# Kernel optimization log

Hardware: AMD Instinct MI355X
Metric: run time of the kernel (lower is better)

## Reference

```python
import jax, jax.numpy as jnp
import numpy as np
from jax import lax

B, H, W, CL, CC, CD, NH, NP = 8, 48, 48, 384, 384, 384, 12, 4
N = H * W
HD = CL // NH
SCALE = HD ** -0.5


def _pool_mat(n, out=7):
    # torch AdaptiveAvgPool2d bin edges: [floor(i*n/out), ceil((i+1)*n/out))
    M = np.zeros((out, n), np.float32)
    for i in range(out):
        s = (i * n) // out
        e = -(-((i + 1) * n) // out)
        M[i, s:e] = 1.0 / (e - s)
    return jnp.asarray(M)


def _resize_mat(out_n, in_n):
    # bilinear, align_corners=False (torch F.interpolate)
    M = np.zeros((out_n, in_n), np.float32)
    scale = in_n / out_n
    for o in range(out_n):
        src = (o + 0.5) * scale - 0.5
        src = min(max(src, 0.0), in_n - 1.0)
        i0 = int(np.floor(src))
        i1 = min(i0 + 1, in_n - 1)
        f = src - i0
        M[o, i0] += 1.0 - f
        M[o, i1] += f
    return jnp.asarray(M)


def _ln_c(x, g, b):
    # LayerNorm over channel dim of NCHW, eps=1e-6
    mu = jnp.mean(x, axis=1, keepdims=True)
    var = jnp.mean((x - mu) ** 2, axis=1, keepdims=True)
    xn = (x - mu) * lax.rsqrt(var + 1e-6)
    return xn * g[None, :, None, None] + b[None, :, None, None]


def _c1(x, w):
    # 1x1 conv, w: (out,in)
    return jnp.einsum('oc,bchw->bohw', w, x)


def _bilerp(feat, grid):
    # feat (G,C,Hs,Ws), grid (G,M,2) xy in [-1,1]; align_corners=False, zero padding
    G, C, Hs, Ws = feat.shape
    x = (grid[..., 0] + 1.0) * 0.5 * Ws - 0.5
    y = (grid[..., 1] + 1.0) * 0.5 * Hs - 0.5
    x0 = jnp.floor(x)
    y0 = jnp.floor(y)
    fx = x - x0
    fy = y - y0
    featf = feat.transpose(0, 2, 3, 1).reshape(G, Hs * Ws, C)
    x0i = x0.astype(jnp.int32)
    y0i = y0.astype(jnp.int32)

    def corner(ix, iy):
        valid = ((ix >= 0) & (ix < Ws) & (iy >= 0) & (iy < Hs)).astype(feat.dtype)
        flat = jnp.clip(iy, 0, Hs - 1) * Ws + jnp.clip(ix, 0, Ws - 1)
        g = jax.vmap(lambda f, i: f[i])(featf, flat)  # (G,M,C)
        return g * valid[..., None]

    v00 = corner(x0i, y0i)
    v01 = corner(x0i + 1, y0i)
    v10 = corner(x0i, y0i + 1)
    v11 = corner(x0i + 1, y0i + 1)
    w00 = ((1 - fx) * (1 - fy))[..., None]
    w01 = (fx * (1 - fy))[..., None]
    w10 = ((1 - fx) * fy)[..., None]
    w11 = (fx * fy)[..., None]
    return v00 * w00 + v01 * w01 + v10 * w10 + v11 * w11  # (G,M,C)


def _forward(local_feat, context_prior, deformable_x, W_q, W_k, W_v, W_pre, ln1_g, ln1_b,
             W_post, dw_w, dw_b, ln2_g, ln2_b, W_lo, b_lo, W_off, b_off,
             attention_biases, W_p, bn_g, bn_b, bn_mean, bn_var):
    q = _c1(local_feat, W_q)  # (B,CL,H,W)

    # context_offset_guide: 1x1 -> GELU -> adaptive pool 7x7 -> LN(C) -> 1x1 to 32 -> resize
    cg = jax.nn.gelu(_c1(context_prior, W_pre), approximate=False)
    Mh, Mw = _pool_mat(H), _pool_mat(W)
    pooled = jnp.einsum('oh,pw,bchw->bcop', Mh, Mw, cg)
    guide = _c1(_ln_c(pooled, ln1_g, ln1_b), W_post)  # (B,32,7,7)
    Uh, Uw = _resize_mat(H, 7), _resize_mat(W, 7)
    guide = jnp.einsum('Oh,Pw,bchw->bcOP', Uh, Uw, guide)  # (B,32,H,W)

    # local_offset_base: dwconv3x3 -> LN(C) -> GELU -> 1x1 to 32
    dw = lax.conv_general_dilated(local_feat, dw_w, (1, 1), [(1, 1), (1, 1)],
                                  dimension_numbers=('NCHW', 'OIHW', 'NCHW'),
                                  feature_group_count=CL) + dw_b[None, :, None, None]
    lo = jax.nn.gelu(_ln_c(dw, ln2_g, ln2_b), approximate=False)
    lo = _c1(lo, W_lo) + b_lo[None, :, None, None]  # (B,32,H,W)

    fused = jnp.concatenate([guide, lo], axis=1)  # (B,64,H,W)
    off = _c1(fused, W_off) + b_off[None, :, None, None]  # (B,NH*NP*2,H,W)
    off = off.transpose(0, 2, 3, 1).reshape(B, H, W, NH, NP, 2)
    offn = off / jnp.asarray([W, H], dtype=off.dtype)

    ry = (jnp.arange(H, dtype=off.dtype) + 0.5) / H
    rx = (jnp.arange(W, dtype=off.dtype) + 0.5) / W
    ref = jnp.stack([jnp.broadcast_to(rx[None, :], (H, W)),
                     jnp.broadcast_to(ry[:, None], (H, W))], axis=-1)  # (H,W,2) xy
    grid = (ref[None, :, :, None, None, :] + offn) * 2.0 - 1.0  # (B,H,W,NH,NP,2)

    gridh = grid.reshape(B, N, NH, NP, 2).transpose(0, 2, 1, 3, 4)  # (B,NH,N,NP,2)
    grid_r = gridh.reshape(B * NH, N * NP, 2)

    k = _c1(context_prior, W_k).reshape(B * NH, HD, H, W)
    v = _c1(deformable_x, W_v).reshape(B * NH, HD, H, W)
    k_s = _bilerp(k, grid_r).reshape(B, NH, N, NP, HD)
    v_s = _bilerp(v, grid_r).reshape(B, NH, N, NP, HD)

    qh = q.reshape(B, NH, HD, N).transpose(0, 1, 3, 2)  # (B,NH,N,HD)
    scores = jnp.einsum('bhnd,bhnpd->bhnp', qh, k_s) * SCALE

    # relative position bias: idx(p1,p2) = |dy|*W + |dx| (first-seen enumeration)
    px = jnp.clip(jnp.round((gridh[..., 0] + 1.0) * 0.5 * W - 0.5), 0, W - 1).astype(jnp.int32)
    py = jnp.clip(jnp.round((gridh[..., 1] + 1.0) * 0.5 * H - 0.5), 0, H - 1).astype(jnp.int32)
    n = jnp.arange(N, dtype=jnp.int32)
    qy = (n // W)[None, None, :, None]
    qx = (n % W)[None, None, :, None]
    bidx = jnp.abs(qy - py) * W + jnp.abs(qx - px)  # (B,NH,N,NP)
    bias = attention_biases[jnp.arange(NH)[None, :, None, None], bidx]

    attn = jax.nn.softmax(scores + bias, axis=-1)
    out = jnp.einsum('bhnp,bhnpd->bhnd', attn, v_s)  # (B,NH,N,HD)
    out = out.transpose(0, 1, 3, 2).reshape(B, CL, H, W)

    y = _c1(out, W_p)
    y = bn_g[None, :, None, None] * (y - bn_mean[None, :, None, None]) * \
        lax.rsqrt(bn_var[None, :, None, None] + 1e-5) + bn_b[None, :, None, None]
    return y


def setup_inputs():
    ks = jax.random.split(jax.random.key(0), 16)
    f32 = jnp.float32
    d = {
        'local_feat': jax.random.normal(ks[0], (B, CL, H, W), f32),
        'context_prior': jax.random.normal(ks[1], (B, CC, H, W), f32),
        'deformable_x': jax.random.normal(ks[2], (B, CD, H, W), f32),
        'W_q': jax.random.normal(ks[3], (CL, CL), f32) * 0.02,
        'W_k': jax.random.normal(ks[4], (CL, CC), f32) * 0.02,
        'W_v': jax.random.normal(ks[5], (CD, CD), f32) * 0.02,
        'W_pre': jax.random.normal(ks[6], (CC, CC), f32) * 0.02,
        'ln1_g': jnp.ones((CC,), f32),
        'ln1_b': jnp.zeros((CC,), f32),
        'W_post': jax.random.normal(ks[7], (32, CC), f32) * 0.02,
        'dw_w': jax.random.normal(ks[8], (CL, 1, 3, 3), f32) * 0.1,
        'dw_b': jnp.zeros((CL,), f32),
        'ln2_g': jnp.ones((CL,), f32),
        'ln2_b': jnp.zeros((CL,), f32),
        'W_lo': jax.random.normal(ks[9], (32, CL), f32) * 0.02,
        'b_lo': jnp.zeros((32,), f32),
        'W_off': jax.random.normal(ks[10], (NH * NP * 2, 64), f32) * 0.01,
        'b_off': jax.random.normal(ks[11], (NH * NP * 2,), f32) * 0.5,
        'attention_biases': jax.random.normal(ks[12], (NH, H * W), f32) * 0.02,
        'W_p': jax.random.normal(ks[13], (CL, CL), f32) * 0.02,
        'bn_g': jnp.ones((CL,), f32),
        'bn_b': jnp.zeros((CL,), f32),
        'bn_mean': jax.random.normal(ks[14], (CL,), f32) * 0.01,
        'bn_var': jax.random.uniform(ks[15], (CL,), f32, 0.5, 1.5),
    }
    return d


def reference(local_feat, context_prior, deformable_x, W_q, W_k, W_v, W_pre, ln1_g, ln1_b,
              W_post, dw_w, dw_b, ln2_g, ln2_b, W_lo, b_lo, W_off, b_off,
              attention_biases, W_p, bn_g, bn_b, bn_mean, bn_var):
    return _forward(local_feat, context_prior, deformable_x, W_q, W_k, W_v, W_pre, ln1_g,
                    ln1_b, W_post, dw_w, dw_b, ln2_g, ln2_b, W_lo, b_lo, W_off, b_off,
                    attention_biases, W_p, bn_g, bn_b, bn_mean, bn_var)
```

## Files before the change

### kernel.cpp

```cpp
#include <hip/hip_runtime.h>
#include <hip/hip_bf16.h>
#include <math.h>

#define B_ 8
#define H_ 48
#define W_ 48
#define N_ 2304
#define C_ 384
#define NH_ 12
#define NP_ 4
#define HD_ 32
#define SCALE_ 0.17677669529663687f

typedef unsigned short ushort;
typedef short bf16x8 __attribute__((ext_vector_type(8)));
typedef float f32x4 __attribute__((ext_vector_type(4)));

__device__ __forceinline__ float b2f(ushort u) {
    union { float f; unsigned i; } x; x.i = ((unsigned)u) << 16; return x.f;
}
__device__ __forceinline__ ushort f2b(float f) {
    __hip_bfloat16 h = __float2bfloat16(f);
    return *(ushort*)&h;
}
__device__ __forceinline__ float ldin(const void* p, size_t i, int isbf) {
    return isbf ? b2f(((const ushort*)p)[i]) : ((const float*)p)[i];
}
__device__ __forceinline__ float geluf(float x) {
    return 0.5f * x * (1.0f + erff(x * 0.70710678118654752440f));
}
__device__ __forceinline__ int iabs(int x) { return x < 0 ? -x : x; }
__device__ __forceinline__ int get_isbf(const void* lnq) {
    return (*(const unsigned*)lnq == 0x3F803F80u) ? 1 : 0;
}

__device__ __forceinline__ void gl_lds16(const ushort* g, ushort* l) {
    __builtin_amdgcn_global_load_lds(
        (const __attribute__((address_space(1))) unsigned int*)g,
        (__attribute__((address_space(3))) unsigned int*)l, 16, 0, 0);
}

#define PREP_MAX 24
struct PrepTab {
    const void* src[PREP_MAX];
    void*       dst[PREP_MAX];
    int         n[PREP_MAX];
    int         tobf[PREP_MAX];
};
struct TPtrs { const void* src[3]; ushort* dst[3]; };
struct SetupRaw {
    const void* WoffRaw;
    const void* WloRaw;
    const void* bloRaw;
    const void* boffRaw;
    const void* dwRaw;
    const void* lnq;
    ushort* Bext;
    float*  biasp;
    float*  dwwT;
};

__global__ __launch_bounds__(256) void setup_kernel(TPtrs tp, PrepTab tab, int ne, SetupRaw rw)
{
    const int isbf = get_isbf(rw.lnq);
    const int tid = threadIdx.x;
    const int bid = blockIdx.x;
    const int DWT0 = ne * 8;
    const int WC0  = DWT0 + 2;
    const int T30  = WC0 + 96;

    if (bid < DWT0) {
        const int e = bid >> 3, sub = bid & 7;
        const int n = tab.n[e];
        const void* src = tab.src[e];
        if (tab.tobf[e]) {
            ushort* dst = (ushort*)tab.dst[e];
            if (isbf) {
                const ushort* s = (const ushort*)src;
                for (int i = sub * 256 + tid; i < n; i += 8 * 256) dst[i] = s[i];
            } else {
                const float* s = (const float*)src;
                for (int i = sub * 256 + tid; i < n; i += 8 * 256) dst[i] = f2b(s[i]);
            }
        } else {
            float* dst = (float*)tab.dst[e];
            if (isbf) {
                const ushort* s = (const ushort*)src;
                for (int i = sub * 256 + tid; i < n; i += 8 * 256) dst[i] = b2f(s[i]);
            } else {
                const float* s = (const float*)src;
                for (int i = sub * 256 + tid; i < n; i += 8 * 256) dst[i] = s[i];
            }
        }
    } else if (bid < WC0) {
        const int c = (bid - DWT0) * 256 + tid;
        if (c < C_) {
#pragma unroll
            for (int u = 0; u < 9; u++)
                rw.dwwT[u * C_ + c] = ldin(rw.dwRaw, (size_t)c * 9 + u, isbf);
        }
    } else if (bid < T30) {
        const int co = bid - WC0;
        const ushort* WoffU = (const ushort*)rw.WoffRaw;
        for (int c = tid; c < C_; c += 256) {
            float acc = 0.f;
#pragma unroll 8
            for (int j = 0; j < 32; j++)
                acc += ldin(rw.WoffRaw, (size_t)co * 64 + 32 + j, isbf)
                     * ldin(rw.WloRaw, (size_t)j * 384 + c, isbf);
            ushort hi = f2b(acc);
            float r = acc - b2f(hi);
            ushort lo = f2b(r);
            rw.Bext[co * 1152 + c] = hi;
            rw.Bext[co * 1152 + 384 + c] = lo;
            rw.Bext[co * 1152 + 768 + c] = hi;
        }
        (void)WoffU;
        if (tid == 0) {
            float bp = ldin(rw.boffRaw, co, isbf);
            for (int j = 0; j < 32; j++)
                bp += ldin(rw.WoffRaw, (size_t)co * 64 + 32 + j, isbf)
                    * ldin(rw.bloRaw, j, isbf);
            rw.biasp[co] = bp;
        }
    } else {
        const int t3 = bid - T30;
        const int x = t3 % 36;
        const int rem = t3 / 36;
        const int y = rem % 12;
        const int z = rem / 12;
        const int which = z >> 3;
        const int b = z & 7;
        const int n0 = x * 64, c0 = y * 32;
        const void* in = tp.src[which];
        ushort* out = tp.dst[which];
        const int t = tid;

        __shared__ unsigned tile[64][33];

        if (isbf) {
            {
                const int c = t >> 3, s = t & 7;
                uint4 v = *(const uint4*)((const ushort*)in + ((size_t)b * C_ + c0 + c) * N_ + n0 + s * 8);
                const int nb = s * 8;
                tile[nb + 0][c] = v.x & 0xffff; tile[nb + 1][c] = v.x >> 16;
                tile[nb + 2][c] = v.y & 0xffff; tile[nb + 3][c] = v.y >> 16;
                tile[nb + 4][c] = v.z & 0xffff; tile[nb + 5][c] = v.z >> 16;
                tile[nb + 6][c] = v.w & 0xffff; tile[nb + 7][c] = v.w >> 16;
            }
            __syncthreads();
            {
                const int n = t >> 2, s = t & 3;
                const int cb = s * 8;
                unsigned p0 = tile[n][cb + 0] | (tile[n][cb + 1] << 16);
                unsigned p1 = tile[n][cb + 2] | (tile[n][cb + 3] << 16);
                unsigned p2 = tile[n][cb + 4] | (tile[n][cb + 5] << 16);
                unsigned p3 = tile[n][cb + 6] | (tile[n][cb + 7] << 16);
                uint4 o; o.x = p0; o.y = p1; o.z = p2; o.w = p3;
                *(uint4*)(out + ((size_t)b * N_ + n0 + n) * C_ + c0 + cb) = o;
            }
        } else {
            float* tf = (float*)&tile[0][0];
            const int tx = t & 31, ty = t >> 5;
            for (int sub = 0; sub < 2; sub++) {
                int ns = n0 + sub * 32;
                __syncthreads();
#pragma unroll
                for (int u = 0; u < 4; u++) {
                    int c = ty + u * 8;
                    tf[c * 33 + tx] = ((const float*)in)[((size_t)b * C_ + c0 + c) * N_ + ns + tx];
                }
                __syncthreads();
#pragma unroll
                for (int u = 0; u < 4; u++) {
                    int n = ty + u * 8;
                    out[((size_t)b * N_ + ns + n) * C_ + c0 + tx] = f2b(tf[tx * 33 + n]);
                }
            }
        }
    }
}

struct QKV4Ptrs { const ushort* A[4]; const ushort* Bw[4]; void* Y[4]; };
__global__ __launch_bounds__(256, 5) void mega_gemm_kernel(
    QKV4Ptrs qp,
    const ushort* __restrict__ AHI, const ushort* __restrict__ ALO,
    const ushort* __restrict__ Bext, float* __restrict__ OFFP)
{
    __shared__ ushort As[2][128 * 32];
    __shared__ ushort Bs[2][128 * 32];
    const int tid = threadIdx.x;
    const int lane = tid & 63, wave = tid >> 6;
    const int wr = wave >> 1, wc = wave & 1;
    const int quad = lane >> 4, l15 = lane & 15;
    const int bid = blockIdx.x;

    if (bid < 432) {
        const int seg = bid % 3;
        const int m0 = (bid / 3) * 128;
        const ushort* Ag = (seg < 2) ? AHI : ALO;
        const int bcol0 = seg * 384;

        f32x4 acc[4][3];
#pragma unroll
        for (int i = 0; i < 4; i++)
#pragma unroll
            for (int j = 0; j < 3; j++) acc[i][j] = (f32x4){0.f, 0.f, 0.f, 0.f};

        auto stage = [&](int p, int kc) {
#pragma unroll
            for (int u = 0; u < 2; u++) {
                int idx = tid + 256 * u;
                int r = idx >> 2, s = idx & 3;
                int rb = r < 96 ? r : 95;
                gl_lds16(Ag + (size_t)(m0 + r) * 384 + kc + 8 * s, &As[p][idx * 8]);
                gl_lds16(Bext + (size_t)rb * 1152 + bcol0 + kc + 8 * s, &Bs[p][idx * 8]);
            }
        };

        stage(0, 0);
        const int nt = 12;
        for (int t = 0; t < nt; ++t) {
            if (t + 1 < nt) {
                stage((t + 1) & 1, (t + 1) * 32);
                asm volatile("s_waitcnt vmcnt(4)" ::: "memory");
            } else {
                asm volatile("s_waitcnt vmcnt(0)" ::: "memory");
            }
            __builtin_amdgcn_s_barrier();
            __builtin_amdgcn_sched_barrier(0);
            const int p = t & 1;
            bf16x8 af[4], bfr[3];
#pragma unroll
            for (int i = 0; i < 4; i++)
                af[i]  = *(const bf16x8*)&As[p][(wr * 64 + i * 16 + l15) * 32 + quad * 8];
#pragma unroll
            for (int j = 0; j < 3; j++)
                bfr[j] = *(const bf16x8*)&Bs[p][(wc * 48 + j * 16 + l15) * 32 + quad * 8];
#pragma unroll
            for (int i = 0; i < 4; i++)
#pragma unroll
                for (int j = 0; j < 3; j++)
                    acc[i][j] = __builtin_amdgcn_mfma_f32_16x16x32_bf16(af[i], bfr[j], acc[i][j], 0, 0, 0);
            __builtin_amdgcn_s_barrier();
        }

        float* out = OFFP + (size_t)seg * ((size_t)B_ * N_ * 96);
#pragma unroll
        for (int i = 0; i < 4; i++) {
#pragma unroll
            for (int r = 0; r < 4; r++) {
                int m = m0 + wr * 64 + i * 16 + quad * 4 + r;
#pragma unroll
                for (int j = 0; j < 3; j++) {
                    int co = wc * 48 + j * 16 + l15;
                    out[(size_t)m * 96 + co] = acc[i][j][r];
                }
            }
        }
    } else {
        const int q = bid - 432;
        const int zc = q / 54, r2 = q % 54;
        const int which = zc >> 3, b = zc & 7;
        const int m0 = (r2 / 3) * 128;
        const int n0 = (r2 % 3) * 128;
        const ushort* Ag = qp.A[which];
        const ushort* Bg = qp.Bw[which];

        f32x4 acc[4][4];
#pragma unroll
        for (int i = 0; i < 4; i++)
#pragma unroll
            for (int j = 0; j < 4; j++) acc[i][j] = (f32x4){0.f, 0.f, 0.f, 0.f};

        const size_t abase = (size_t)b * (size_t)N_ * C_;

        auto stage = [&](int p, int kc) {
#pragma unroll
            for (int u = 0; u < 2; u++) {
                int idx = tid + 256 * u;
                int r = idx >> 2, s = idx & 3;
                gl_lds16(Ag + abase + (size_t)(m0 + r) * C_ + kc + 8 * s, &As[p][idx * 8]);
                gl_lds16(Bg + (size_t)(n0 + r) * C_ + kc + 8 * s, &Bs[p][idx * 8]);
            }
        };

        stage(0, 0);
        const int nt = C_ / 32;
        for (int t = 0; t < nt; ++t) {
            if (t + 1 < nt) {
                stage((t + 1) & 1, (t + 1) * 32);
                asm volatile("s_waitcnt vmcnt(4)" ::: "memory");
            } else {
                asm volatile("s_waitcnt vmcnt(0)" ::: "memory");
            }
            __builtin_amdgcn_s_barrier();
            __builtin_amdgcn_sched_barrier(0);
            const int p = t & 1;
            bf16x8 af[4], bfr[4];
#pragma unroll
            for (int i = 0; i < 4; i++)
                af[i]  = *(const bf16x8*)&As[p][(wr * 64 + i * 16 + l15) * 32 + quad * 8];
#pragma unroll
            for (int j = 0; j < 4; j++)
                bfr[j] = *(const bf16x8*)&Bs[p][(wc * 64 + j * 16 + l15) * 32 + quad * 8];
#pragma unroll
            for (int i = 0; i < 4; i++)
#pragma unroll
                for (int j = 0; j < 4; j++)
                    acc[i][j] = __builtin_amdgcn_mfma_f32_16x16x32_bf16(af[i], bfr[j], acc[i][j], 0, 0, 0);
            __builtin_amdgcn_s_barrier();
        }

        if (which < 3) {
            ushort* Yg = (ushort*)qp.Y[which];
#pragma unroll
            for (int i = 0; i < 4; i++) {
#pragma unroll
                for (int r = 0; r < 4; r++) {
                    int m = m0 + wr * 64 + i * 16 + quad * 4 + r;
#pragma unroll
                    for (int j = 0; j < 4; j++) {
                        int nn = n0 + wc * 64 + j * 16 + l15;
                        Yg[abase + (size_t)m * C_ + nn] = f2b(acc[i][j][r]);
                    }
                }
            }
        } else {
            float* Yg = (float*)qp.Y[3];
#pragma unroll
            for (int i = 0; i < 4; i++) {
#pragma unroll
                for (int r = 0; r < 4; r++) {
                    int m = m0 + wr * 64 + i * 16 + quad * 4 + r;
#pragma unroll
                    for (int j = 0; j < 4; j++) {
                        int nn = n0 + wc * 64 + j * 16 + l15;
                        Yg[abase + (size_t)m * C_ + nn] = geluf(acc[i][j][r]);
                    }
                }
            }
        }
    }
}

__global__ __launch_bounds__(256) void gemm_final_kernel(
    const ushort* __restrict__ WpB, const ushort* __restrict__ AOut,
    void* __restrict__ Yg,
    const float* __restrict__ bng, const float* __restrict__ bnb,
    const float* __restrict__ bnm, const float* __restrict__ bnv,
    const void* __restrict__ lnq)
{
    const int isbf = get_isbf(lnq);
    const int l = (blockIdx.x & 7) * 108 + (blockIdx.x >> 3);
    const int b = l / 108, r2 = l % 108;
    const int n0 = (r2 / 3) * 64;
    const int m0 = (r2 % 3) * 128;

    __shared__ ushort As[2][128 * 32];
    __shared__ ushort Bs[2][64 * 32];
    const int tid = threadIdx.x;
    const int lane = tid & 63, wave = tid >> 6;
    const int quad = lane >> 4, l15 = lane & 15;
    const int sx = (quad ^ (l15 & 3)) * 8;

    f32x4 acc[2][4];
#pragma unroll
    for (int i = 0; i < 2; i++)
#pragma unroll
        for (int j = 0; j < 4; j++) acc[i][j] = (f32x4){0.f, 0.f, 0.f, 0.f};

    const size_t bbase = (size_t)b * (size_t)N_ * C_;

    auto stage = [&](int p, int kc) {
#pragma unroll
        for (int u = 0; u < 2; u++) {
            int idx = tid + 256 * u;
            int r = idx >> 2, sl = idx & 3;
            int sg = sl ^ (r & 3);
            gl_lds16(WpB + (size_t)(m0 + r) * C_ + kc + 8 * sg, &As[p][idx * 8]);
        }
        {
            int r = tid >> 2, sl = tid & 3;
            int sg = sl ^ (r & 3);
            gl_lds16(AOut + bbase + (size_t)(n0 + r) * C_ + kc + 8 * sg, &Bs[p][tid * 8]);
        }
    };

    stage(0, 0);

    const int nt = C_ / 32;
    for (int t = 0; t < nt; ++t) {
        if (t + 1 < nt) {
            stage((t + 1) & 1, (t + 1) * 32);
            asm volatile("s_waitcnt vmcnt(3)" ::: "memory");
        } else {
            asm volatile("s_waitcnt vmcnt(0)" ::: "memory");
        }
        __builtin_amdgcn_s_barrier();
        __builtin_amdgcn_sched_barrier(0);
        const int p = t & 1;
        bf16x8 af[2], bfr[4];
#pragma unroll
        for (int i = 0; i < 2; i++)
            af[i]  = *(const bf16x8*)&As[p][(wave * 32 + i * 16 + l15) * 32 + sx];
#pragma unroll
        for (int j = 0; j < 4; j++)
            bfr[j] = *(const bf16x8*)&Bs[p][(j * 16 + l15) * 32 + sx];
#pragma unroll
        for (int i = 0; i < 2; i++)
#pragma unroll
            for (int j = 0; j < 4; j++)
                acc[i][j] = __builtin_amdgcn_mfma_f32_16x16x32_bf16(af[i], bfr[j], acc[i][j], 0, 0, 0);
        __builtin_amdgcn_s_barrier();
    }

    const size_t ybase = (size_t)b * (size_t)C_ * N_;
#pragma unroll
    for (int i = 0; i < 2; i++) {
#pragma unroll
        for (int r = 0; r < 4; r++) {
            int m = m0 + wave * 32 + i * 16 + quad * 4 + r;
            float sc = bng[m] * rsqrtf(bnv[m] + 1e-5f);
            float sh = bnb[m] - sc * bnm[m];
#pragma unroll
            for (int j = 0; j < 4; j++) {
                int nn = n0 + j * 16 + l15;
                float v = sc * acc[i][j][r] + sh;
                size_t yi = ybase + (size_t)m * N_ + nn;
                if (isbf) ((ushort*)Yg)[yi] = f2b(v);
                else ((float*)Yg)[yi] = v;
            }
        }
    }
}

__global__ __launch_bounds__(384) void pool_ln_guide_kernel(
    const float* __restrict__ CG, const float* __restrict__ g, const float* __restrict__ bt,
    const ushort* __restrict__ WpostB, const ushort* __restrict__ WoffB,
    float* __restrict__ OG7)
{
    const int cell = blockIdx.x % 49, b = blockIdx.x / 49;
    const int i = cell / 7, j = cell % 7, c = threadIdx.x;
    const int sh = (i * H_) / 7, eh = ((i + 1) * H_ + 6) / 7;
    const int sw = (j * W_) / 7, ew = ((j + 1) * W_ + 6) / 7;
    float s = 0.f;
    for (int h = sh; h < eh; h++)
        for (int w = sw; w < ew; w++)
            s += CG[((size_t)b * N_ + h * W_ + w) * C_ + c];
    s *= 1.0f / (float)((eh - sh) * (ew - sw));

    float rs = s, rq = s * s;
#pragma unroll
    for (int m = 1; m <= 32; m <<= 1) {
        rs += __shfl_xor(rs, m);
        rq += __shfl_xor(rq, m);
    }
    __shared__ float ss[6], sq[6], buf[C_];
    __shared__ float psum[12][33];
    __shared__ float g7s[32];
    int wid = threadIdx.x >> 6;
    if ((threadIdx.x & 63) == 0) { ss[wid] = rs; sq[wid] = rq; }
    __syncthreads();
    if (threadIdx.x == 0) {
        float ts = 0.f, tq = 0.f;
        for (int k = 0; k < 6; k++) { ts += ss[k]; tq += sq[k]; }
        ss[0] = ts; sq[0] = tq;
    }
    __syncthreads();
    float mu = ss[0] / (float)C_;
    float var = sq[0] / (float)C_ - mu * mu;
    float inv = rsqrtf(var + 1e-6f);
    buf[c] = (s - mu) * inv * g[c] + bt[c];
    __syncthreads();

    const int oc = threadIdx.x & 31, seg = threadIdx.x >> 5;
    const uint4* wp = (const uint4*)(WpostB + oc * C_ + seg * 32);
    float part = 0.f;
#pragma unroll
    for (int u = 0; u < 4; u++) {
        uint4 v = wp[u];
        const float* bb = &buf[seg * 32 + u * 8];
        part += b2f((ushort)(v.x & 0xffff)) * bb[0] + b2f((ushort)(v.x >> 16)) * bb[1];
        part += b2f((ushort)(v.y & 0xffff)) * bb[2] + b2f((ushort)(v.y >> 16)) * bb[3];
        part += b2f((ushort)(v.z & 0xffff)) * bb[4] + b2f((ushort)(v.z >> 16)) * bb[5];
        part += b2f((ushort)(v.w & 0xffff)) * bb[6] + b2f((ushort)(v.w >> 16)) * bb[7];
    }
    psum[seg][oc] = part;
    __syncthreads();
    if (threadIdx.x < 32) {
        float acc = 0.f;
#pragma unroll
        for (int k = 0; k < 12; k++) acc += psum[k][threadIdx.x];
        g7s[threadIdx.x] = acc;
    }
    __syncthreads();
    if (threadIdx.x < 96) {
        const int co = threadIdx.x;
        float acc = 0.f;
#pragma unroll 8
        for (int k = 0; k < 32; k++)
            acc += b2f(WoffB[co * 64 + k]) * g7s[k];
        OG7[(size_t)blockIdx.x * 96 + co] = acc;
    }
}

__global__ __launch_bounds__(512) void dw_ln_gelu_kernel(
    const ushort* __restrict__ LF, const float* __restrict__ WdT, const float* __restrict__ BdF,
    const float* __restrict__ g, const float* __restrict__ bt,
    ushort* __restrict__ AHI, ushort* __restrict__ ALO)
{
    const int wave = threadIdx.x >> 6, lane = threadIdx.x & 63;
    const int m = blockIdx.x * 8 + wave;
    const int b = m / N_, n = m % N_;
    const int h = n / W_, w = n % W_;
    const bool act = lane < 48;
    const int c0 = lane * 8;

    float acc[8];
#pragma unroll
    for (int j = 0; j < 8; j++) acc[j] = 0.f;
    if (act) {
        f32x4 b0 = *(const f32x4*)(BdF + c0);
        f32x4 b1 = *(const f32x4*)(BdF + c0 + 4);
#pragma unroll
        for (int j = 0; j < 4; j++) { acc[j] = b0[j]; acc[4 + j] = b1[j]; }
    }

#pragma unroll
    for (int u = 0; u < 9; u++) {
        const int ky = u / 3, kx = u % 3;
        const int y = h + ky - 1, x = w + kx - 1;
        if (act && y >= 0 && y < H_ && x >= 0 && x < W_) {
            uint4 v = *(const uint4*)(LF + ((size_t)b * N_ + y * W_ + x) * C_ + c0);
            f32x4 wa = *(const f32x4*)(WdT + u * C_ + c0);
            f32x4 wb = *(const f32x4*)(WdT + u * C_ + c0 + 4);
            acc[0] += wa[0] * b2f((ushort)(v.x & 0xffff));
            acc[1] += wa[1] * b2f((ushort)(v.x >> 16));
            acc[2] += wa[2] * b2f((ushort)(v.y & 0xffff));
            acc[3] += wa[3] * b2f((ushort)(v.y >> 16));
            acc[4] += wb[0] * b2f((ushort)(v.z & 0xffff));
            acc[5] += wb[1] * b2f((ushort)(v.z >> 16));
            acc[6] += wb[2] * b2f((ushort)(v.w & 0xffff));
            acc[7] += wb[3] * b2f((ushort)(v.w >> 16));
        }
    }

    float rs = 0.f, rq = 0.f;
#pragma unroll
    for (int j = 0; j < 8; j++) { rs += acc[j]; rq += acc[j] * acc[j]; }
#pragma unroll
    for (int s = 1; s <= 32; s <<= 1) {
        rs += __shfl_xor(rs, s);
        rq += __shfl_xor(rq, s);
    }
    float mu = rs / (float)C_;
    float var = rq / (float)C_ - mu * mu;
    float inv = rsqrtf(var + 1e-6f);

    if (act) {
        f32x4 g0 = *(const f32x4*)(g + c0);
        f32x4 g1 = *(const f32x4*)(g + c0 + 4);
        f32x4 t0 = *(const f32x4*)(bt + c0);
        f32x4 t1 = *(const f32x4*)(bt + c0 + 4);
        float v[8];
#pragma unroll
        for (int j = 0; j < 4; j++) {
            v[j]     = geluf((acc[j]     - mu) * inv * g0[j] + t0[j]);
            v[4 + j] = geluf((acc[4 + j] - mu) * inv * g1[j] + t1[j]);
        }
        uint4 hi, lo;
        ushort hs[8], ls[8];
#pragma unroll
        for (int j = 0; j < 8; j++) {
            hs[j] = f2b(v[j]);
            ls[j] = f2b(v[j] - b2f(hs[j]));
        }
        hi.x = (unsigned)hs[0] | ((unsigned)hs[1] << 16);
        hi.y = (unsigned)hs[2] | ((unsigned)hs[3] << 16);
        hi.z = (unsigned)hs[4] | ((unsigned)hs[5] << 16);
        hi.w = (unsigned)hs[6] | ((unsigned)hs[7] << 16);
        lo.x = (unsigned)ls[0] | ((unsigned)ls[1] << 16);
        lo.y = (unsigned)ls[2] | ((unsigned)ls[3] << 16);
        lo.z = (unsigned)ls[4] | ((unsigned)ls[5] << 16);
        lo.w = (unsigned)ls[6] | ((unsigned)ls[7] << 16);
        size_t idx = (size_t)m * C_ + c0;
        *(uint4*)(AHI + idx) = hi;
        *(uint4*)(ALO + idx) = lo;
    }
}

__global__ __launch_bounds__(384) void attn_kernel(
    const ushort* __restrict__ Q, const ushort* __restrict__ K, const ushort* __restrict__ V,
    const float* __restrict__ OFFP, const float* __restrict__ biasp,
    const float* __restrict__ OG7,
    const float* __restrict__ ABf, ushort* __restrict__ OUT)
{
    const int pairi = blockIdx.x;
    const int b = pairi / (N_ / 2);
    const int n0 = (pairi % (N_ / 2)) * 2;
    const int tid = threadIdx.x;

    __shared__ int   cidxS[96][4];
    __shared__ float cwS[96][4];
    __shared__ float biasS[96];

    if (tid < 96) {
        const int pos = tid / 48, idx = tid % 48;
        const int n = n0 + pos;
        const int h = n / W_, w = n % W_;
        const int nh = idx >> 2, p = idx & 3;
        const int co = nh * 8 + 2 * p;

        const float fs = 7.0f / 48.0f;
        float sy = fminf(fmaxf(((float)h + 0.5f) * fs - 0.5f, 0.f), 6.f);
        float sx = fminf(fmaxf(((float)w + 0.5f) * fs - 0.5f, 0.f), 6.f);
        int gy0 = (int)floorf(sy), gx0 = (int)floorf(sx);
        int gy1 = min(gy0 + 1, 6), gx1 = min(gx0 + 1, 6);
        float gfy = sy - (float)gy0, gfx = sx - (float)gx0;
        float bw00 = (1.f - gfy) * (1.f - gfx), bw01 = (1.f - gfy) * gfx;
        float bw10 = gfy * (1.f - gfx), bw11 = gfy * gfx;
        const float* ogb = OG7 + (size_t)b * 49 * 96;
        int c00 = (gy0 * 7 + gx0) * 96, c01 = (gy0 * 7 + gx1) * 96;
        int c10 = (gy1 * 7 + gx0) * 96, c11 = (gy1 * 7 + gx1) * 96;
        const size_t MS = (size_t)B_ * N_ * 96;
        const size_t mrow = ((size_t)b * N_ + n) * 96;

        float ox = OFFP[mrow + co] + OFFP[MS + mrow + co] + OFFP[2 * MS + mrow + co]
                 + biasp[co]
                 + bw00 * ogb[c00 + co] + bw01 * ogb[c01 + co]
                 + bw10 * ogb[c10 + co] + bw11 * ogb[c11 + co];
        float oy = OFFP[mrow + co + 1] + OFFP[MS + mrow + co + 1] + OFFP[2 * MS + mrow + co + 1]
                 + biasp[co + 1]
                 + bw00 * ogb[c00 + co + 1] + bw01 * ogb[c01 + co + 1]
                 + bw10 * ogb[c10 + co + 1] + bw11 * ogb[c11 + co + 1];

        float x = (float)w + ox;
        float y = (float)h + oy;

        int px = (int)fminf(fmaxf(rintf(x), 0.f), (float)(W_ - 1));
        int py = (int)fminf(fmaxf(rintf(y), 0.f), (float)(H_ - 1));
        biasS[tid] = ABf[(size_t)nh * N_ + iabs(h - py) * W_ + iabs(w - px)];

        float x0f = floorf(x), y0f = floorf(y);
        float fx = x - x0f, fy = y - y0f;
        int x0 = (int)x0f, y0 = (int)y0f;
#pragma unroll
        for (int cc = 0; cc < 4; cc++) {
            int dx = cc & 1, dy = cc >> 1;
            int ix = x0 + dx, iy = y0 + dy;
            bool valid = (ix >= 0) && (ix < W_) && (iy >= 0) && (iy < H_);
            int ixc = min(max(ix, 0), W_ - 1), iyc = min(max(iy, 0), H_ - 1);
            cidxS[tid][cc] = iyc * W_ + ixc;
            float wx = dx ? fx : (1.f - fx);
            float wy = dy ? fy : (1.f - fy);
            cwS[tid][cc] = valid ? wx * wy : 0.f;
        }
    }
    __syncthreads();

    const int pos = tid / 192, r = tid % 192;
    const int nh = r >> 4, dd = r & 15;
    const int n = n0 + pos;
    const size_t row = ((size_t)b * N_ + n) * C_ + nh * HD_ + dd * 2;
    unsigned qu = *(const unsigned*)(Q + row);
    const float q0 = b2f((ushort)(qu & 0xffff));
    const float q1 = b2f((ushort)(qu >> 16));
    const size_t kvbase = (size_t)b * N_ * C_ + nh * HD_ + dd * 2;
    const int s0 = pos * 48 + nh * 4;

    int   ci[NP_][4];
    float cw[NP_][4];
#pragma unroll
    for (int p = 0; p < NP_; p++)
#pragma unroll
        for (int cc = 0; cc < 4; cc++) {
            ci[p][cc] = cidxS[s0 + p][cc];
            cw[p][cc] = cwS[s0 + p][cc];
        }

    float sc[NP_];
#pragma unroll
    for (int p = 0; p < NP_; p++) {
        float ks0 = 0.f, ks1 = 0.f;
#pragma unroll
        for (int cc = 0; cc < 4; cc++) {
            unsigned kv = *(const unsigned*)(K + kvbase + (size_t)ci[p][cc] * C_);
            ks0 += cw[p][cc] * b2f((ushort)(kv & 0xffff));
            ks1 += cw[p][cc] * b2f((ushort)(kv >> 16));
        }
        float dot = q0 * ks0 + q1 * ks1;
#pragma unroll
        for (int m = 1; m <= 8; m <<= 1) dot += __shfl_xor(dot, m);
        sc[p] = dot * SCALE_ + biasS[s0 + p];
    }

    float m = fmaxf(fmaxf(sc[0], sc[1]), fmaxf(sc[2], sc[3]));
    float e[NP_], esum = 0.f;
#pragma unroll
    for (int p = 0; p < NP_; p++) { e[p] = __expf(sc[p] - m); esum += e[p]; }
    float inv = 1.0f / esum;

    float o0 = 0.f, o1 = 0.f;
#pragma unroll
    for (int p = 0; p < NP_; p++) {
        float vs0 = 0.f, vs1 = 0.f;
#pragma unroll
        for (int cc = 0; cc < 4; cc++) {
            unsigned vv = *(const unsigned*)(V + kvbase + (size_t)ci[p][cc] * C_);
            vs0 += cw[p][cc] * b2f((ushort)(vv & 0xffff));
            vs1 += cw[p][cc] * b2f((ushort)(vv >> 16));
        }
        float ep = e[p] * inv;
        o0 += ep * vs0;
        o1 += ep * vs1;
    }
    unsigned ou = (unsigned)f2b(o0) | ((unsigned)f2b(o1) << 16);
    *(unsigned*)(OUT + row) = ou;
}

extern "C" void kernel_launch(void* const* d_in, const int* in_sizes, int n_in,
                              void* d_out, int out_size, void* d_ws, size_t ws_size,
                              hipStream_t stream)
{
    const void* local_feat    = d_in[0];
    const void* context_prior = d_in[1];
    const void* deformable_x  = d_in[2];

    const size_t BIGE = (size_t)B_ * N_ * C_;

    char* wsb = (char*)d_ws;
    auto carve = [&](size_t bytes) { char* p = wsb; wsb += (bytes + 255) & ~(size_t)255; return p; };
    int*    flag = (int*)carve(256);
    ushort* T1   = (ushort*)carve(BIGE * 2);
    ushort* T2   = (ushort*)carve(BIGE * 2);
    ushort* T3   = (ushort*)carve(BIGE * 2);
    ushort* Qb   = (ushort*)carve(BIGE * 2);
    ushort* Kb   = (ushort*)carve(BIGE * 2);
    ushort* Vb   = (ushort*)carve(BIGE * 2);
    ushort* AHI  = (ushort*)carve(BIGE * 2);
    ushort* ALO  = (ushort*)carve(BIGE * 2);
    float*  CGR  = (float*)carve(BIGE * 4);
    float*  OFFB = (float*)carve((size_t)B_ * N_ * 96 * 4 * 3);
    ushort* WqB   = (ushort*)carve(147456 * 2);
    ushort* WkB   = (ushort*)carve(147456 * 2);
    ushort* WvB   = (ushort*)carve(147456 * 2);
    ushort* WpreB = (ushort*)carve(147456 * 2);
    ushort* WpB   = (ushort*)carve(147456 * 2);
    ushort* WpostB= (ushort*)carve(12288 * 2);
    ushort* WoffB = (ushort*)carve(6144 * 2);
    ushort* Bext  = (ushort*)carve(96 * 1152 * 2);
    float*  biasp = (float*)carve(96 * 4);
    float*  OG7   = (float*)carve((size_t)B_ * 49 * 96 * 4);
    float*  dwwT  = (float*)carve(3456 * 4);
    float*  ABf   = (float*)carve(27648 * 4);
    float*  dwbF  = (float*)carve(384 * 4);
    float*  ln1gF = (float*)carve(384 * 4);
    float*  ln1bF = (float*)carve(384 * 4);
    float*  ln2gF = (float*)carve(384 * 4);
    float*  ln2bF = (float*)carve(384 * 4);
    float*  bngF  = (float*)carve(384 * 4);
    float*  bnbF  = (float*)carve(384 * 4);
    float*  bnmF  = (float*)carve(384 * 4);
    float*  bnvF  = (float*)carve(384 * 4);
    ushort* AOut = (ushort*)CGR + BIGE;
    (void)flag;

    PrepTab tab;
    int ne = 0;
    auto add = [&](const void* s, void* d, int n, int tb) {
        tab.src[ne] = s; tab.dst[ne] = d; tab.n[ne] = n; tab.tobf[ne] = tb; ne++;
    };
    add(d_in[3],  WqB,   147456, 1);
    add(d_in[4],  WkB,   147456, 1);
    add(d_in[5],  WvB,   147456, 1);
    add(d_in[6],  WpreB, 147456, 1);
    add(d_in[19], WpB,   147456, 1);
    add(d_in[9],  WpostB, 12288, 1);
    add(d_in[16], WoffB,   6144, 1);
    add(d_in[18], ABf,    27648, 0);
    add(d_in[11], dwbF,     384, 0);
    add(d_in[7],  ln1gF,    384, 0);
    add(d_in[8],  ln1bF,    384, 0);
    add(d_in[12], ln2gF,    384, 0);
    add(d_in[13], ln2bF,    384, 0);
    add(d_in[20], bngF,     384, 0);
    add(d_in[21], bnbF,     384, 0);
    add(d_in[22], bnmF,     384, 0);
    add(d_in[23], bnvF,     384, 0);

    TPtrs tp;
    tp.src[0] = local_feat;    tp.dst[0] = T1;
    tp.src[1] = context_prior; tp.dst[1] = T2;
    tp.src[2] = deformable_x;  tp.dst[2] = T3;

    SetupRaw rw;
    rw.WoffRaw = d_in[16];
    rw.WloRaw  = d_in[14];
    rw.bloRaw  = d_in[15];
    rw.boffRaw = d_in[17];
    rw.dwRaw   = d_in[10];
    rw.lnq     = d_in[7];
    rw.Bext    = Bext;
    rw.biasp   = biasp;
    rw.dwwT    = dwwT;

    const int setup_blocks = ne * 8 + 2 + 96 + 10368;
    setup_kernel<<<setup_blocks, 256, 0, stream>>>(tp, tab, ne, rw);

    dim3 blk256(256);

    dw_ln_gelu_kernel<<<(B_ * N_) / 8, 512, 0, stream>>>(T1, dwwT, dwbF, ln2gF, ln2bF, AHI, ALO);

    QKV4Ptrs qp;
    qp.A[0] = T1; qp.Bw[0] = WqB;   qp.Y[0] = Qb;
    qp.A[1] = T2; qp.Bw[1] = WkB;   qp.Y[1] = Kb;
    qp.A[2] = T3; qp.Bw[2] = WvB;   qp.Y[2] = Vb;
    qp.A[3] = T2; qp.Bw[3] = WpreB; qp.Y[3] = CGR;
    mega_gemm_kernel<<<2160, blk256, 0, stream>>>(qp, AHI, ALO, Bext, OFFB);

    pool_ln_guide_kernel<<<B_ * 49, 384, 0, stream>>>(CGR, ln1gF, ln1bF, WpostB, WoffB, OG7);

    attn_kernel<<<(B_ * N_) / 2, 384, 0, stream>>>(Qb, Kb, Vb, OFFB, biasp, OG7, ABf, AOut);

    gemm_final_kernel<<<864, blk256, 0, stream>>>(
        WpB, AOut, d_out, bngF, bnbF, bnmF, bnvF, d_in[7]);
}
```

Before: 344.6 us.

## Fuse offset GEMM split-K segments in-block and store GELU context as bf16

```diff
diff --git a/kernel.cpp b/kernel.cpp
--- a/kernel.cpp
+++ b/kernel.cpp
@@ -101,7 +101,6 @@
         }
     } else if (bid < T30) {
         const int co = bid - WC0;
-        const ushort* WoffU = (const ushort*)rw.WoffRaw;
         for (int c = tid; c < C_; c += 256) {
             float acc = 0.f;
 #pragma unroll 8
@@ -115,7 +114,6 @@
             rw.Bext[co * 1152 + 384 + c] = lo;
             rw.Bext[co * 1152 + 768 + c] = hi;
         }
-        (void)WoffU;
         if (tid == 0) {
             float bp = ldin(rw.boffRaw, co, isbf);
             for (int j = 0; j < 32; j++)
@@ -195,11 +193,8 @@
     const int quad = lane >> 4, l15 = lane & 15;
     const int bid = blockIdx.x;
 
-    if (bid < 432) {
-        const int seg = bid % 3;
-        const int m0 = (bid / 3) * 128;
-        const ushort* Ag = (seg < 2) ? AHI : ALO;
-        const int bcol0 = seg * 384;
+    if (bid < 144) {
+        const int m0 = bid * 128;
 
         f32x4 acc[4][3];
 #pragma unroll
@@ -207,22 +202,26 @@
 #pragma unroll
             for (int j = 0; j < 3; j++) acc[i][j] = (f32x4){0.f, 0.f, 0.f, 0.f};
 
-        auto stage = [&](int p, int kc) {
+        auto stage = [&](int p, int t) {
+            const int seg = t / 12;
+            const ushort* Ag = (seg < 2) ? AHI : ALO;
+            const int acol = t * 32 - seg * 384;
+            const int bcol = t * 32;
 #pragma unroll
             for (int u = 0; u < 2; u++) {
                 int idx = tid + 256 * u;
                 int r = idx >> 2, s = idx & 3;
                 int rb = r < 96 ? r : 95;
-                gl_lds16(Ag + (size_t)(m0 + r) * 384 + kc + 8 * s, &As[p][idx * 8]);
-                gl_lds16(Bext + (size_t)rb * 1152 + bcol0 + kc + 8 * s, &Bs[p][idx * 8]);
+                gl_lds16(Ag + (size_t)(m0 + r) * 384 + acol + 8 * s, &As[p][idx * 8]);
+                gl_lds16(Bext + (size_t)rb * 1152 + bcol + 8 * s, &Bs[p][idx * 8]);
             }
         };
 
         stage(0, 0);
-        const int nt = 12;
+        const int nt = 36;
         for (int t = 0; t < nt; ++t) {
             if (t + 1 < nt) {
-                stage((t + 1) & 1, (t + 1) * 32);
+                stage((t + 1) & 1, t + 1);
                 asm volatile("s_waitcnt vmcnt(4)" ::: "memory");
             } else {
                 asm volatile("s_waitcnt vmcnt(0)" ::: "memory");
@@ -245,7 +244,6 @@
             __builtin_amdgcn_s_barrier();
         }
 
-        float* out = OFFP + (size_t)seg * ((size_t)B_ * N_ * 96);
 #pragma unroll
         for (int i = 0; i < 4; i++) {
 #pragma unroll
@@ -254,12 +252,12 @@
 #pragma unroll
                 for (int j = 0; j < 3; j++) {
                     int co = wc * 48 + j * 16 + l15;
-                    out[(size_t)m * 96 + co] = acc[i][j][r];
+                    OFFP[(size_t)m * 96 + co] = acc[i][j][r];
                 }
             }
         }
     } else {
-        const int q = bid - 432;
+        const int q = bid - 144;
         const int zc = q / 54, r2 = q % 54;
         const int which = zc >> 3, b = zc & 7;
         const int m0 = (r2 / 3) * 128;
@@ -312,8 +310,8 @@
             __builtin_amdgcn_s_barrier();
         }
 
+        ushort* Yg = (ushort*)qp.Y[which];
         if (which < 3) {
-            ushort* Yg = (ushort*)qp.Y[which];
 #pragma unroll
             for (int i = 0; i < 4; i++) {
 #pragma unroll
@@ -327,7 +325,6 @@
                 }
             }
         } else {
-            float* Yg = (float*)qp.Y[3];
 #pragma unroll
             for (int i = 0; i < 4; i++) {
 #pragma unroll
@@ -336,7 +333,7 @@
 #pragma unroll
                     for (int j = 0; j < 4; j++) {
                         int nn = n0 + wc * 64 + j * 16 + l15;
-                        Yg[abase + (size_t)m * C_ + nn] = geluf(acc[i][j][r]);
+                        Yg[abase + (size_t)m * C_ + nn] = f2b(geluf(acc[i][j][r]));
                     }
                 }
             }
@@ -436,7 +433,7 @@
 }
 
 __global__ __launch_bounds__(384) void pool_ln_guide_kernel(
-    const float* __restrict__ CG, const float* __restrict__ g, const float* __restrict__ bt,
+    const ushort* __restrict__ CG, const float* __restrict__ g, const float* __restrict__ bt,
     const ushort* __restrict__ WpostB, const ushort* __restrict__ WoffB,
     float* __restrict__ OG7)
 {
@@ -447,7 +444,7 @@
     float s = 0.f;
     for (int h = sh; h < eh; h++)
         for (int w = sw; w < ew; w++)
-            s += CG[((size_t)b * N_ + h * W_ + w) * C_ + c];
+            s += b2f(CG[((size_t)b * N_ + h * W_ + w) * C_ + c]);
     s *= 1.0f / (float)((eh - sh) * (ew - sw));
 
     float rs = s, rq = s * s;
@@ -623,15 +620,12 @@
         const float* ogb = OG7 + (size_t)b * 49 * 96;
         int c00 = (gy0 * 7 + gx0) * 96, c01 = (gy0 * 7 + gx1) * 96;
         int c10 = (gy1 * 7 + gx0) * 96, c11 = (gy1 * 7 + gx1) * 96;
-        const size_t MS = (size_t)B_ * N_ * 96;
         const size_t mrow = ((size_t)b * N_ + n) * 96;
 
-        float ox = OFFP[mrow + co] + OFFP[MS + mrow + co] + OFFP[2 * MS + mrow + co]
-                 + biasp[co]
+        float ox = OFFP[mrow + co] + biasp[co]
                  + bw00 * ogb[c00 + co] + bw01 * ogb[c01 + co]
                  + bw10 * ogb[c10 + co] + bw11 * ogb[c11 + co];
-        float oy = OFFP[mrow + co + 1] + OFFP[MS + mrow + co + 1] + OFFP[2 * MS + mrow + co + 1]
-                 + biasp[co + 1]
+        float oy = OFFP[mrow + co + 1] + biasp[co + 1]
                  + bw00 * ogb[c00 + co + 1] + bw01 * ogb[c01 + co + 1]
                  + bw10 * ogb[c10 + co + 1] + bw11 * ogb[c11 + co + 1];
 
@@ -740,8 +734,9 @@
     ushort* Vb   = (ushort*)carve(BIGE * 2);
     ushort* AHI  = (ushort*)carve(BIGE * 2);
     ushort* ALO  = (ushort*)carve(BIGE * 2);
-    float*  CGR  = (float*)carve(BIGE * 4);
-    float*  OFFB = (float*)carve((size_t)B_ * N_ * 96 * 4 * 3);
+    ushort* CGB  = (ushort*)carve(BIGE * 2);
+    ushort* AOut = (ushort*)carve(BIGE * 2);
+    float*  OFFB = (float*)carve((size_t)B_ * N_ * 96 * 4);
     ushort* WqB   = (ushort*)carve(147456 * 2);
     ushort* WkB   = (ushort*)carve(147456 * 2);
     ushort* WvB   = (ushort*)carve(147456 * 2);
@@ -763,7 +758,6 @@
     float*  bnbF  = (float*)carve(384 * 4);
     float*  bnmF  = (float*)carve(384 * 4);
     float*  bnvF  = (float*)carve(384 * 4);
-    ushort* AOut = (ushort*)CGR + BIGE;
     (void)flag;
 
     PrepTab tab;
@@ -816,10 +810,10 @@
     qp.A[0] = T1; qp.Bw[0] = WqB;   qp.Y[0] = Qb;
     qp.A[1] = T2; qp.Bw[1] = WkB;   qp.Y[1] = Kb;
     qp.A[2] = T3; qp.Bw[2] = WvB;   qp.Y[2] = Vb;
-    qp.A[3] = T2; qp.Bw[3] = WpreB; qp.Y[3] = CGR;
-    mega_gemm_kernel<<<2160, blk256, 0, stream>>>(qp, AHI, ALO, Bext, OFFB);
-
-    pool_ln_guide_kernel<<<B_ * 49, 384, 0, stream>>>(CGR, ln1gF, ln1bF, WpostB, WoffB, OG7);
+    qp.A[3] = T2; qp.Bw[3] = WpreB; qp.Y[3] = CGB;
+    mega_gemm_kernel<<<1872, blk256, 0, stream>>>(qp, AHI, ALO, Bext, OFFB);
+
+    pool_ln_guide_kernel<<<B_ * 49, 384, 0, stream>>>(CGB, ln1gF, ln1bF, WpostB, WoffB, OG7);
 
     attn_kernel<<<(B_ * N_) / 2, 384, 0, stream>>>(Qb, Kb, Vb, OFFB, biasp, OG7, ABf, AOut);
 
```

Result: no change. 344.5 us (-0.0%).
